# Kernel tuning notes

Measured on AMD Instinct MI355X. Metric: run time of the kernel, lower is better.

The kernel has to match this reference:

```python
import jax, jax.numpy as jnp
import numpy as np

B, BARS, BEATS, FRAC = 64, 16, 4, 8
IN_F = 10 * 47 * 2  # 940
LIN_OUT = 100
BEAT_H = 16
BAR_H = 32


def _p(key, shape, scale=0.05):
    return jax.random.normal(key, shape, dtype=jnp.float32) * scale


def setup_inputs() -> dict:
    key = jax.random.key(0)
    ks = jax.random.split(key, 16)
    return {
        "channels": jax.random.normal(ks[0], (B, BARS, BEATS, FRAC, 10, 2, 47), dtype=jnp.float32),
        "lin_w": _p(ks[1], (LIN_OUT, IN_F)),
        "lin_b": _p(ks[2], (LIN_OUT,)),
        # beats LSTM (unidirectional), PyTorch gate order i,f,g,o
        "b_wih": _p(ks[3], (4 * BEAT_H, LIN_OUT)),
        "b_whh": _p(ks[4], (4 * BEAT_H, BEAT_H)),
        "b_bih": _p(ks[5], (4 * BEAT_H,)),
        "b_bhh": _p(ks[6], (4 * BEAT_H,)),
        # bars LSTM, bidirectional: forward (f_) and reverse (r_) directions
        "f_wih": _p(ks[7], (4 * BAR_H, BEAT_H)),
        "f_whh": _p(ks[8], (4 * BAR_H, BAR_H)),
        "f_bih": _p(ks[9], (4 * BAR_H,)),
        "f_bhh": _p(ks[10], (4 * BAR_H,)),
        "r_wih": _p(ks[11], (4 * BAR_H, BEAT_H)),
        "r_whh": _p(ks[12], (4 * BAR_H, BAR_H)),
        "r_bih": _p(ks[13], (4 * BAR_H,)),
        "r_bhh": _p(ks[14], (4 * BAR_H,)),
    }


def lstm(x, wih, whh, bih, bhh):
    """PyTorch-semantics LSTM, batch_first. x: [N, T, F] -> h_seq [N, T, H]."""
    N = x.shape[0]
    H = whh.shape[1]
    # precompute input contribution for all timesteps
    xg = jnp.einsum('ntf,gf->ntg', x, wih) + (bih + bhh)  # [N, T, 4H]

    def step(carry, xt):
        h, c = carry
        gates = xt + h @ whh.T  # [N, 4H]
        i, f, g, o = jnp.split(gates, 4, axis=-1)
        c = jax.nn.sigmoid(f) * c + jax.nn.sigmoid(i) * jnp.tanh(g)
        h = jax.nn.sigmoid(o) * jnp.tanh(c)
        return (h, c), h

    h0 = jnp.zeros((N, H), x.dtype)
    _, hs = jax.lax.scan(step, (h0, h0), jnp.swapaxes(xg, 0, 1))  # [T, N, H]
    return jnp.swapaxes(hs, 0, 1)


def bilstm(x, f_wih, f_whh, f_bih, f_bhh, r_wih, r_whh, r_bih, r_bhh):
    fwd = lstm(x, f_wih, f_whh, f_bih, f_bhh)
    bwd = jnp.flip(lstm(jnp.flip(x, axis=1), r_wih, r_whh, r_bih, r_bhh), axis=1)
    return jnp.concatenate([fwd, bwd], axis=-1)


def reference(channels, lin_w, lin_b,
              b_wih, b_whh, b_bih, b_bhh,
              f_wih, f_whh, f_bih, f_bhh,
              r_wih, r_whh, r_bih, r_bhh):
    # channels: [B, bars, beats, frac, 10, 2, 47]
    x = jnp.swapaxes(channels, -1, -2)  # [..., 10, 47, 2]
    x = x.reshape(*x.shape[:4], IN_F)   # squash dims 4..6 -> 940
    x = jax.nn.relu(x @ lin_w.T + lin_b)  # [B, bars, beats, frac, 100]

    # Distributed depth=2: fold (B, bars, beats) into batch, seq over frac
    xb = x.reshape(B * BARS * BEATS, FRAC, LIN_OUT)
    beats = lstm(xb, b_wih, b_whh, b_bih, b_bhh)
    beats = beats.reshape(B, BARS, BEATS, FRAC, BEAT_H)

    # last fraction hidden state, then Distributed depth=1 over beats axis
    xl = beats[:, :, :, -1].reshape(B * BARS, BEATS, BEAT_H)
    bars = bilstm(xl, f_wih, f_whh, f_bih, f_bhh, r_wih, r_whh, r_bih, r_bhh)
    bars = bars.reshape(B, BARS, BEATS, 2 * BAR_H)
    return beats, bars
```

## Files before the change

### kernel.cpp

```cpp
#include <hip/hip_runtime.h>
#include <hip/hip_bf16.h>

typedef float f32x4 __attribute__((ext_vector_type(4)));
typedef short bf16x8 __attribute__((ext_vector_type(8)));

#define MFMA16(a, b, c) __builtin_amdgcn_mfma_f32_16x16x32_bf16(a, b, c, 0, 0, 0)

constexpr int K1  = 940;
constexpr int KP2 = 1024;
constexpr int NP  = 112;
constexpr int OSL = 136;
constexpr int BSR = 136;
constexpr int BUFE = NP * BSR;

__device__ __forceinline__ float sigf(float x) { return 1.f / (1.f + __expf(-x)); }
__device__ __forceinline__ float tanhfast(float x) { return 2.f / (1.f + __expf(-2.f * x)) - 1.f; }

__device__ __forceinline__ short f2b(float x) {
  __hip_bfloat16 b = __float2bfloat16(x);
  return *reinterpret_cast<short*>(&b);
}

__device__ __forceinline__ void lds_barrier() {
  asm volatile("s_waitcnt lgkmcnt(0)" ::: "memory");
  __builtin_amdgcn_s_barrier();
  __builtin_amdgcn_sched_barrier(0);
}

__global__ void prep_kernel(const float* __restrict__ lin_w,
                            const float* __restrict__ b_wih,
                            __hip_bfloat16* __restrict__ w2,
                            __hip_bfloat16* __restrict__ bw2) {
  int idx = blockIdx.x * 256 + threadIdx.x;
  if (idx < NP * KP2) {
    int n = idx >> 10, k = idx & 1023;
    float v = 0.f;
    if (n < 100 && k < K1) {
      int c10 = k / 94, rem = k - c10 * 94;
      int c2 = rem / 47, c47 = rem - c2 * 47;
      int f = c10 * 94 + c47 * 2 + c2;
      v = lin_w[n * K1 + f];
    }
    w2[idx] = __float2bfloat16(v);
  } else {
    int i2 = idx - NP * KP2;
    if (i2 < 64 * 128) {
      int g = i2 >> 7, k = i2 & 127;
      bw2[i2] = __float2bfloat16((k < 100) ? b_wih[g * 100 + k] : 0.f);
    }
  }
}

__global__ __launch_bounds__(256, 2)
void fused_encoder(const float* __restrict__ ch,
                   const __hip_bfloat16* __restrict__ w2,
                   const float* __restrict__ lin_b,
                   const __hip_bfloat16* __restrict__ bw2,
                   const float* __restrict__ bih,
                   const float* __restrict__ bhh,
                   const float* __restrict__ whh,
                   const float* __restrict__ fwih, const float* __restrict__ fwhh,
                   const float* __restrict__ fbih, const float* __restrict__ fbhh,
                   const float* __restrict__ rwih, const float* __restrict__ rwhh,
                   const float* __restrict__ rbih, const float* __restrict__ rbhh,
                   float* __restrict__ beats,
                   float* __restrict__ bars) {
  __shared__ __align__(16) char smem[2 * BUFE * 2];
  __hip_bfloat16* Bs    = reinterpret_cast<__hip_bfloat16*>(smem);
  __hip_bfloat16* out_s = reinterpret_cast<__hip_bfloat16*>(smem);
  float*          xg_s  = reinterpret_cast<float*>(smem + 17408);
  float (*hlast)[16]    = reinterpret_cast<float(*)[16]>(smem + 34048);
  float (*hb)[32]       = reinterpret_cast<float(*)[32]>(smem + 34560);
  float (*gact)[128]    = reinterpret_cast<float(*)[128]>(smem + 34816);

  const int tid = threadIdx.x;
  const int w = tid >> 6, lane = tid & 63;
  const int l16 = lane & 15, bq = lane >> 4;

  const int mbase = blockIdx.x * 64 + w * 16;
  const float* ar = ch + (long)(mbase + l16) * K1 + bq * 8;

  float lb[7];
#pragma unroll
  for (int nt = 0; nt < 7; ++nt) {
    int col = nt * 16 + l16;
    lb[nt] = (col < 100) ? lin_b[col] : 0.f;
  }

  auto mk = [&](float4 lo, float4 hi) -> bf16x8 {
    return bf16x8{f2b(lo.x), f2b(lo.y), f2b(lo.z), f2b(lo.w),
                  f2b(hi.x), f2b(hi.y), f2b(hi.z), f2b(hi.w)};
  };

  f32x4 acc[7] = {};
  float4 Ab[3][8];
  bf16x8 bst[8];

  const float4 f40{0.f, 0.f, 0.f, 0.f};
  auto ldA = [&](int c, float4* d) {
    const float* p = ar + c * 128;
    if (c < 7) {
#pragma unroll
      for (int ks = 0; ks < 4; ++ks) {
        d[2 * ks]     = *reinterpret_cast<const float4*>(p + ks * 32);
        d[2 * ks + 1] = *reinterpret_cast<const float4*>(p + ks * 32 + 4);
      }
    } else {
      d[0] = *reinterpret_cast<const float4*>(p);
      d[1] = *reinterpret_cast<const float4*>(p + 4);
      d[2] = (bq <= 1) ? *reinterpret_cast<const float4*>(p + 32) : f40;
      d[3] = (bq == 0) ? *reinterpret_cast<const float4*>(p + 36) : f40;
      d[4] = d[5] = d[6] = d[7] = f40;
    }
  };

  const int sn = tid >> 1, kh = (tid & 1) * 64;
  auto stageB_ld = [&](int c) {
    if (sn < NP) {
      const __hip_bfloat16* src = w2 + sn * KP2 + c * 128 + kh;
#pragma unroll
      for (int j = 0; j < 8; ++j)
        bst[j] = *reinterpret_cast<const bf16x8*>(src + j * 8);
    }
  };
  auto stageB_st = [&](int buf) {
    if (sn < NP) {
      __hip_bfloat16* dst = Bs + buf * BUFE + sn * BSR + kh;
#pragma unroll
      for (int j = 0; j < 8; ++j)
        *reinterpret_cast<bf16x8*>(dst + j * 8) = bst[j];
    }
  };

  stageB_ld(0);
  ldA(0, Ab[0]);
  ldA(1, Ab[1]);
  stageB_st(0);
  lds_barrier();

#pragma unroll
  for (int c = 0; c < 8; ++c) {
    if (c < 7) stageB_ld(c + 1);
    if (c < 6) ldA(c + 2, Ab[(c + 2) % 3]);
    const __hip_bfloat16* Bc = Bs + (c & 1) * BUFE;
    float4* A = Ab[c % 3];
#pragma unroll
    for (int ks = 0; ks < 4; ++ks) {
      bf16x8 bf[7];
#pragma unroll
      for (int nt = 0; nt < 7; ++nt)
        bf[nt] = *reinterpret_cast<const bf16x8*>(
            &Bc[(nt * 16 + l16) * BSR + ks * 32 + bq * 8]);
      bf16x8 a = mk(A[2 * ks], A[2 * ks + 1]);
#pragma unroll
      for (int nt = 0; nt < 7; ++nt) acc[nt] = MFMA16(a, bf[nt], acc[nt]);
    }
    if (c < 7) stageB_st((c + 1) & 1);
    lds_barrier();
  }

#pragma unroll
  for (int nt = 0; nt < 7; ++nt) {
    const int col = nt * 16 + l16;
#pragma unroll
    for (int r = 0; r < 4; ++r) {
      float v = fmaxf(acc[nt][r] + lb[nt], 0.f);
      out_s[(w * 16 + bq * 4 + r) * OSL + col] = __float2bfloat16((col < 100) ? v : 0.f);
    }
  }
#pragma unroll
  for (int r = 0; r < 4; ++r)
    out_s[(w * 16 + bq * 4 + r) * OSL + 112 + l16] = __float2bfloat16(0.f);

  {
    bf16x8 av[4];
#pragma unroll
    for (int s = 0; s < 4; ++s)
      av[s] = *reinterpret_cast<const bf16x8*>(&out_s[(w * 16 + l16) * OSL + s * 32 + bq * 8]);
    f32x4 xacc[4] = {};
#pragma unroll
    for (int gt = 0; gt < 4; ++gt) {
#pragma unroll
      for (int s = 0; s < 4; ++s) {
        bf16x8 b = *reinterpret_cast<const bf16x8*>(&bw2[(gt * 16 + l16) * 128 + s * 32 + bq * 8]);
        xacc[gt] = MFMA16(av[s], b, xacc[gt]);
      }
    }
#pragma unroll
    for (int gt = 0; gt < 4; ++gt) {
      const int gate = gt * 16 + l16;
      const float bias = bih[gate] + bhh[gate];
#pragma unroll
      for (int r = 0; r < 4; ++r)
        xg_s[(w * 16 + bq * 4 + r) * 65 + gate] = xacc[gt][r] + bias;
    }
  }

  {
    const int cell = lane & 15;
    float wr[16];
#pragma unroll
    for (int u = 0; u < 16; ++u) wr[u] = whh[lane * 16 + u];
    float xv0[8], xv1[8];
#pragma unroll
    for (int t = 0; t < 8; ++t) {
      xv0[t] = xg_s[(w * 16 + t) * 65 + lane];
      xv1[t] = xg_s[(w * 16 + 8 + t) * 65 + lane];
    }
    float h0[16], h1[16];
#pragma unroll
    for (int u = 0; u < 16; ++u) { h0[u] = 0.f; h1[u] = 0.f; }
    float c0 = 0.f, c1 = 0.f;
    const long sg0 = (long)blockIdx.x * 8 + 2 * w;
    const long sg1 = sg0 + 1;
#pragma unroll
    for (int t = 0; t < 8; ++t) {
      float p0 = xv0[t], p1 = xv1[t];
#pragma unroll
      for (int u = 0; u < 16; ++u) { p0 += wr[u] * h0[u]; p1 += wr[u] * h1[u]; }
      const bool istanh = (lane >= 32 && lane < 48);
      float a0 = istanh ? tanhfast(p0) : sigf(p0);
      float a1 = istanh ? tanhfast(p1) : sigf(p1);
      float gi0 = __shfl(a0, cell),      gi1 = __shfl(a1, cell);
      float gf0 = __shfl(a0, cell + 16), gf1 = __shfl(a1, cell + 16);
      float gg0 = __shfl(a0, cell + 32), gg1 = __shfl(a1, cell + 32);
      float go0 = __shfl(a0, cell + 48), go1 = __shfl(a1, cell + 48);
      c0 = gf0 * c0 + gi0 * gg0;
      c1 = gf1 * c1 + gi1 * gg1;
      float hn0 = go0 * tanhfast(c0);
      float hn1 = go1 * tanhfast(c1);
#pragma unroll
      for (int u = 0; u < 16; ++u) { h0[u] = __shfl(hn0, u); h1[u] = __shfl(hn1, u); }
      if (lane < 16) {
        beats[sg0 * 128 + t * 16 + lane] = hn0;
        beats[sg1 * 128 + t * 16 + lane] = hn1;
        if (t == 7) {
          hlast[2 * w][lane]     = hn0;
          hlast[2 * w + 1][lane] = hn1;
        }
      }
    }
  }
  __syncthreads();

  {
    const int dir = tid >> 7, g = tid & 127;
    const float* wihp = dir ? rwih : fwih;
    const float* whhp = dir ? rwhh : fwhh;
    const float bias = dir ? (rbih[g] + rbhh[g]) : (fbih[g] + fbhh[g]);
    float wi[16], wh[32];
#pragma unroll
    for (int u = 0; u < 16; ++u) wi[u] = wihp[g * 16 + u];
#pragma unroll
    for (int u = 0; u < 32; ++u) wh[u] = whhp[g * 32 + u];
    for (int b2 = 0; b2 < 2; ++b2) {
      const int n = blockIdx.x * 2 + b2;
      float c = 0.f;
      if (g < 32) hb[dir][g] = 0.f;
      __syncthreads();
      for (int t = 0; t < 4; ++t) {
        const int tt = dir ? (3 - t) : t;
        float pre = bias;
#pragma unroll
        for (int u = 0; u < 16; ++u) pre += wi[u] * hlast[b2 * 4 + tt][u];
#pragma unroll
        for (int u = 0; u < 32; ++u) pre += wh[u] * hb[dir][u];
        gact[dir][g] = (g >= 64 && g < 96) ? tanhfast(pre) : sigf(pre);
        __syncthreads();
        if (g < 32) {
          c = gact[dir][32 + g] * c + gact[dir][g] * gact[dir][64 + g];
          float hn = gact[dir][96 + g] * tanhfast(c);
          hb[dir][g] = hn;
          bars[(n * 4 + tt) * 64 + dir * 32 + g] = hn;
        }
        __syncthreads();
      }
    }
  }
}

extern "C" void kernel_launch(void* const* d_in, const int* in_sizes, int n_in,
                              void* d_out, int out_size, void* d_ws, size_t ws_size,
                              hipStream_t stream) {
  const float* ch    = (const float*)d_in[0];
  const float* lin_w = (const float*)d_in[1];
  const float* lin_b = (const float*)d_in[2];
  const float* b_wih = (const float*)d_in[3];
  const float* b_whh = (const float*)d_in[4];
  const float* b_bih = (const float*)d_in[5];
  const float* b_bhh = (const float*)d_in[6];
  const float* f_wih = (const float*)d_in[7];
  const float* f_whh = (const float*)d_in[8];
  const float* f_bih = (const float*)d_in[9];
  const float* f_bhh = (const float*)d_in[10];
  const float* r_wih = (const float*)d_in[11];
  const float* r_whh = (const float*)d_in[12];
  const float* r_bih = (const float*)d_in[13];
  const float* r_bhh = (const float*)d_in[14];

  char* ws = (char*)d_ws;
  __hip_bfloat16* w2  = (__hip_bfloat16*)ws;
  __hip_bfloat16* bw2 = (__hip_bfloat16*)(ws + 229376);
  float*          out = (float*)d_out;

  prep_kernel<<<480, 256, 0, stream>>>(lin_w, b_wih, w2, bw2);
  fused_encoder<<<512, 256, 0, stream>>>(ch, w2, lin_b, bw2, b_bih, b_bhh,
                                         b_whh,
                                         f_wih, f_whh, f_bih, f_bhh,
                                         r_wih, r_whh, r_bih, r_bhh,
                                         out, out + 524288);
}
```

Measured before the change: 230.1 us.

## Stage A tile through swizzled LDS with coalesced loads, single-buffer B

The input activations (A) were read directly into registers with a strided per-lane pattern and converted to bf16 at use. They are now loaded with row-contiguous, coalesced float4 reads, converted to bf16 once and stored into an XOR-swizzled LDS tile. B is stored with the same swizzle instead of padded rows, and its double buffer becomes a single buffer with two barriers per chunk. Coalesced global reads and fewer LDS bank conflicts are traded for less prefetch depth and extra synchronisation.

After: 231.4 us. About the same (+0.6%).

```diff
diff --git a/kernel.cpp b/kernel.cpp
--- a/kernel.cpp
+++ b/kernel.cpp
@@ -3,6 +3,7 @@
 
 typedef float f32x4 __attribute__((ext_vector_type(4)));
 typedef short bf16x8 __attribute__((ext_vector_type(8)));
+typedef short bf16x4 __attribute__((ext_vector_type(4)));
 
 #define MFMA16(a, b, c) __builtin_amdgcn_mfma_f32_16x16x32_bf16(a, b, c, 0, 0, 0)
 
@@ -10,8 +11,6 @@
 constexpr int KP2 = 1024;
 constexpr int NP  = 112;
 constexpr int OSL = 136;
-constexpr int BSR = 136;
-constexpr int BUFE = NP * BSR;
 
 __device__ __forceinline__ float sigf(float x) { return 1.f / (1.f + __expf(-x)); }
 __device__ __forceinline__ float tanhfast(float x) { return 2.f / (1.f + __expf(-2.f * x)) - 1.f; }
@@ -65,8 +64,9 @@
                    const float* __restrict__ rbih, const float* __restrict__ rbhh,
                    float* __restrict__ beats,
                    float* __restrict__ bars) {
-  __shared__ __align__(16) char smem[2 * BUFE * 2];
-  __hip_bfloat16* Bs    = reinterpret_cast<__hip_bfloat16*>(smem);
+  __shared__ __align__(16) char smem[45056];
+  char* As = smem;
+  char* Bw = smem + 16384;
   __hip_bfloat16* out_s = reinterpret_cast<__hip_bfloat16*>(smem);
   float*          xg_s  = reinterpret_cast<float*>(smem + 17408);
   float (*hlast)[16]    = reinterpret_cast<float(*)[16]>(smem + 34048);
@@ -77,9 +77,6 @@
   const int w = tid >> 6, lane = tid & 63;
   const int l16 = lane & 15, bq = lane >> 4;
 
-  const int mbase = blockIdx.x * 64 + w * 16;
-  const float* ar = ch + (long)(mbase + l16) * K1 + bq * 8;
-
   float lb[7];
 #pragma unroll
   for (int nt = 0; nt < 7; ++nt) {
@@ -87,75 +84,79 @@
     lb[nt] = (col < 100) ? lin_b[col] : 0.f;
   }
 
-  auto mk = [&](float4 lo, float4 hi) -> bf16x8 {
-    return bf16x8{f2b(lo.x), f2b(lo.y), f2b(lo.z), f2b(lo.w),
-                  f2b(hi.x), f2b(hi.y), f2b(hi.z), f2b(hi.w)};
+  f32x4 acc[7] = {};
+  float4 rA[8];
+  bf16x8 bst[8];
+
+  const float4 f40{0.f, 0.f, 0.f, 0.f};
+
+  const int acolf = (lane & 31) * 4;
+  const float* asrc = ch + (long)(blockIdx.x * 64 + w * 16 + (lane >> 5)) * K1 + acolf;
+  auto ldA = [&](int c) {
+    const float* p = asrc + c * 128;
+    if (c < 7) {
+#pragma unroll
+      for (int j = 0; j < 8; ++j)
+        rA[j] = *reinterpret_cast<const float4*>(p + (long)j * 2 * K1);
+    } else {
+      const bool ok = acolf < 44;
+#pragma unroll
+      for (int j = 0; j < 8; ++j)
+        rA[j] = ok ? *reinterpret_cast<const float4*>(p + (long)j * 2 * K1) : f40;
+    }
   };
-
-  f32x4 acc[7] = {};
-  float4 Ab[3][8];
-  bf16x8 bst[8];
-
-  const float4 f40{0.f, 0.f, 0.f, 0.f};
-  auto ldA = [&](int c, float4* d) {
-    const float* p = ar + c * 128;
-    if (c < 7) {
-#pragma unroll
-      for (int ks = 0; ks < 4; ++ks) {
-        d[2 * ks]     = *reinterpret_cast<const float4*>(p + ks * 32);
-        d[2 * ks + 1] = *reinterpret_cast<const float4*>(p + ks * 32 + 4);
-      }
-    } else {
-      d[0] = *reinterpret_cast<const float4*>(p);
-      d[1] = *reinterpret_cast<const float4*>(p + 4);
-      d[2] = (bq <= 1) ? *reinterpret_cast<const float4*>(p + 32) : f40;
-      d[3] = (bq == 0) ? *reinterpret_cast<const float4*>(p + 36) : f40;
-      d[4] = d[5] = d[6] = d[7] = f40;
+  auto stA = [&]() {
+#pragma unroll
+    for (int j = 0; j < 8; ++j) {
+      const int row = w * 16 + (lane >> 5) + 2 * j;
+      const int byte = row * 256 + (((lane & 31) * 8) ^ ((row & 7) << 4));
+      bf16x4 v = {f2b(rA[j].x), f2b(rA[j].y), f2b(rA[j].z), f2b(rA[j].w)};
+      *reinterpret_cast<bf16x4*>(As + byte) = v;
     }
   };
 
-  const int sn = tid >> 1, kh = (tid & 1) * 64;
-  auto stageB_ld = [&](int c) {
+  const int sn = tid >> 1;
+  const int khb = (tid & 1) * 128;
+  auto ldB = [&](int c) {
     if (sn < NP) {
-      const __hip_bfloat16* src = w2 + sn * KP2 + c * 128 + kh;
+      const __hip_bfloat16* src = w2 + sn * KP2 + c * 128 + (tid & 1) * 64;
 #pragma unroll
       for (int j = 0; j < 8; ++j)
         bst[j] = *reinterpret_cast<const bf16x8*>(src + j * 8);
     }
   };
-  auto stageB_st = [&](int buf) {
+  auto stB = [&]() {
     if (sn < NP) {
-      __hip_bfloat16* dst = Bs + buf * BUFE + sn * BSR + kh;
+      const int swz = (sn & 7) << 4;
 #pragma unroll
       for (int j = 0; j < 8; ++j)
-        *reinterpret_cast<bf16x8*>(dst + j * 8) = bst[j];
+        *reinterpret_cast<bf16x8*>(Bw + sn * 256 + ((khb + j * 16) ^ swz)) = bst[j];
     }
   };
 
-  stageB_ld(0);
-  ldA(0, Ab[0]);
-  ldA(1, Ab[1]);
-  stageB_st(0);
-  lds_barrier();
+  ldA(0);
+  ldB(0);
+
+  const int fsw = (l16 & 7) << 4;
+  const int abase = (w * 16 + l16) * 256;
 
 #pragma unroll
   for (int c = 0; c < 8; ++c) {
-    if (c < 7) stageB_ld(c + 1);
-    if (c < 6) ldA(c + 2, Ab[(c + 2) % 3]);
-    const __hip_bfloat16* Bc = Bs + (c & 1) * BUFE;
-    float4* A = Ab[c % 3];
+    stA();
+    stB();
+    lds_barrier();
+    if (c < 7) { ldA(c + 1); ldB(c + 1); }
 #pragma unroll
     for (int ks = 0; ks < 4; ++ks) {
-      bf16x8 bf[7];
-#pragma unroll
-      for (int nt = 0; nt < 7; ++nt)
-        bf[nt] = *reinterpret_cast<const bf16x8*>(
-            &Bc[(nt * 16 + l16) * BSR + ks * 32 + bq * 8]);
-      bf16x8 a = mk(A[2 * ks], A[2 * ks + 1]);
-#pragma unroll
-      for (int nt = 0; nt < 7; ++nt) acc[nt] = MFMA16(a, bf[nt], acc[nt]);
-    }
-    if (c < 7) stageB_st((c + 1) & 1);
+      const int ko = (ks * 64 + bq * 16);
+      bf16x8 a = *reinterpret_cast<const bf16x8*>(As + abase + (ko ^ fsw));
+#pragma unroll
+      for (int nt = 0; nt < 7; ++nt) {
+        bf16x8 b = *reinterpret_cast<const bf16x8*>(
+            Bw + (nt * 16 + l16) * 256 + (ko ^ fsw));
+        acc[nt] = MFMA16(a, b, acc[nt]);
+      }
+    }
     lds_barrier();
   }
 
```
